# Kernel optimization log

Hardware: AMD Instinct MI355X
Metric: run time of the kernel (lower is better)

The kernel has to match this reference:

```python
import jax, jax.numpy as jnp
import numpy as np

N, E, IN_DIM, OUT_DIM, H = 4096, 131072, 1024, 512, 4


def setup_inputs() -> dict:
    key = jax.random.key(0)
    k1, k2, k3, k4 = jax.random.split(key, 4)
    x = jax.random.normal(k1, (N, IN_DIM), dtype=jnp.float32)
    edge_index = jax.random.randint(k2, (2, E), 0, N, dtype=jnp.int64)
    # learned params, scaled like torch Linear init (~1/sqrt(fan_in))
    W = jax.random.normal(k3, (H, IN_DIM, OUT_DIM), dtype=jnp.float32) * 0.02
    a = jax.random.normal(k4, (H, 2 * OUT_DIM), dtype=jnp.float32) * 0.02
    return {"x": x, "edge_index": edge_index, "W": W, "a": a}


def reference(x, edge_index, W, a):
    row, col = edge_index[0], edge_index[1]
    n = x.shape[0]
    h = jnp.einsum('ni,hio->hno', x, W)                    # [H, N, out]
    # per-edge attention logits: a . [h[row] || h[col]]
    a_src, a_dst = a[:, :OUT_DIM], a[:, OUT_DIM:]
    e = (jnp.einsum('heo,ho->he', h[:, row], a_src)
         + jnp.einsum('heo,ho->he', h[:, col], a_dst))      # [H, E]
    e = jnp.where(e > 0, e, 0.2 * e)                        # LeakyReLU(0.2)
    # dense NxN attention matrix exactly as the original (zeros at non-edges
    # DO participate in the row softmax, matching the torch code)
    att = jnp.zeros((H, n, n), dtype=h.dtype).at[:, row, col].set(e)
    att = jax.nn.softmax(att, axis=-1)
    h_prime = jnp.einsum('hnm,hmo->hno', att, h)            # [H, N, out]
    return jnp.transpose(h_prime, (1, 0, 2)).reshape(n, H * OUT_DIM)
```

## Files before the change

### kernel.cpp

```cpp
#include <hip/hip_runtime.h>
#include <stdint.h>

#define NN 4096
#define EE 131072
#define IND 1024
#define OUTD 512
#define NH 4
#define NBKT 8
#define BKT_SHIFT 9

typedef __bf16 bf16x8 __attribute__((ext_vector_type(8)));
typedef float f32x4 __attribute__((ext_vector_type(4)));
typedef float f32x2 __attribute__((ext_vector_type(2)));

__device__ __forceinline__ unsigned short f2bf(float f) {
  unsigned u = __float_as_uint(f);
  u += 0x7FFFu + ((u >> 16) & 1u);
  return (unsigned short)(u >> 16);
}

__global__ void prep_edge_kernel(const float* __restrict__ x, unsigned short* __restrict__ xb,
                                 const float* __restrict__ W, unsigned short* __restrict__ Wt,
                                 const int* __restrict__ ei, unsigned* __restrict__ bitmap,
                                 int* __restrict__ counts2, unsigned char* __restrict__ flags) {
  __shared__ float tile[32][33];
  const int bid = blockIdx.x, t = threadIdx.x;
  if (bid < 4096) {
    int i = bid * 256 + t;
    float4 v = ((const float4*)x)[i];
    ushort4 o;
    o.x = f2bf(v.x); o.y = f2bf(v.y); o.z = f2bf(v.z); o.w = f2bf(v.w);
    ((ushort4*)xb)[i] = o;
  } else if (bid < 6144) {
    int b2 = bid - 4096;
    int i0 = (b2 & 31) * 32, o0 = ((b2 >> 5) & 15) * 32, h = b2 >> 9;
    int tx = t & 31, ty = t >> 5;
#pragma unroll
    for (int r = 0; r < 32; r += 8)
      tile[ty + r][tx] = W[((size_t)(h * IND + i0 + ty + r)) * OUTD + o0 + tx];
    __syncthreads();
#pragma unroll
    for (int r = 0; r < 32; r += 8)
      Wt[((size_t)(h * OUTD + o0 + ty + r)) * IND + i0 + tx] = f2bf(tile[tx][ty + r]);
  } else {
    int e = (bid - 6144) * 256 + t;
    int row = ei[e], col = ei[EE + e];
    unsigned key = ((unsigned)row << 12) | (unsigned)col;
    unsigned bit = 1u << (key & 31);
    unsigned old = atomicOr(&bitmap[key >> 5], bit);
    if (old & bit) { flags[e] = 1; return; }
    flags[e] = 0;
    atomicAdd(&counts2[row * NBKT + (col >> BKT_SHIFT)], 1);
  }
}

__device__ __forceinline__ void gload16(const unsigned short* g, unsigned short* l) {
  __builtin_amdgcn_global_load_lds((const __attribute__((address_space(1))) void*)g,
                                   (__attribute__((address_space(3))) void*)l, 16, 0, 0);
}

__device__ void scan_block_256(const int* __restrict__ c2, int* __restrict__ off2,
                               int* __restrict__ cur2) {
  __shared__ int wtot[4];
  const int t = threadIdx.x, w = t >> 6, lane = t & 63;
  const int4* src = (const int4*)c2 + t * 32;
  int s = 0;
  for (int k = 0; k < 32; k++) { int4 v = src[k]; s += v.x + v.y + v.z + v.w; }
  int inc = s;
#pragma unroll
  for (int d = 1; d < 64; d <<= 1) {
    int u = __shfl_up(inc, d);
    if (lane >= d) inc += u;
  }
  if (lane == 63) wtot[w] = inc;
  __syncthreads();
  int wpre = 0;
#pragma unroll
  for (int k = 0; k < 4; k++)
    if (k < w) wpre += wtot[k];
  int o = wpre + inc - s;
  if (t == 255) off2[NN * NBKT] = o + s;
  int4* od = (int4*)off2 + t * 32;
  int4* cd = (int4*)cur2 + t * 32;
  for (int k = 0; k < 32; k++) {
    int4 v = src[k];
    int4 ov;
    ov.x = o; o += v.x;
    ov.y = o; o += v.y;
    ov.z = o; o += v.z;
    ov.w = o; o += v.w;
    od[k] = ov;
    cd[k] = ov;
  }
}

__global__ __launch_bounds__(256, 4) void gemm_scan_kernel(
    const unsigned short* __restrict__ X, const unsigned short* __restrict__ Wt,
    const float* __restrict__ Av, unsigned char* __restrict__ Hb8,
    float* __restrict__ s4_src, float* __restrict__ s4_dst, float* __restrict__ Scol,
    const int* __restrict__ c2, int* __restrict__ off2, int* __restrict__ cur2) {
  if (blockIdx.x == 512) {
    scan_block_256(c2, off2, cur2);
    return;
  }
  __shared__ __align__(16) unsigned short As[2][4096];
  __shared__ __align__(16) unsigned short Bs[2][4096];
  const int t = threadIdx.x, w = t >> 6, lane = t & 63;
  const int bx = blockIdx.x & 3, hh = (blockIdx.x >> 2) & 3, by = blockIdx.x >> 4;

  const unsigned short* Ab0 = X + (size_t)(by * 128) * IND;
  const unsigned short* Bb0 = Wt + (size_t)(hh * OUTD + bx * 128) * IND;

  const int seg0 = w * 128 + lane, seg1 = w * 128 + 64 + lane;
  const int sr0 = seg0 >> 2, sc0 = (seg0 & 3) ^ ((sr0 >> 1) & 3);
  const int sr1 = seg1 >> 2, sc1 = (seg1 & 3) ^ ((sr1 >> 1) & 3);

  const int wr = w >> 1, wc = w & 1, g = lane >> 4, rlo = lane & 15;
  int aoff[4], boff[4];
#pragma unroll
  for (int i = 0; i < 4; i++) {
    int ra = wr * 64 + i * 16 + rlo;
    aoff[i] = ra * 64 + ((g ^ ((ra >> 1) & 3)) << 4);
    int rb = wc * 64 + i * 16 + rlo;
    boff[i] = rb * 64 + ((g ^ ((rb >> 1) & 3)) << 4);
  }

  f32x4 zero = {0.f, 0.f, 0.f, 0.f};
  f32x4 acc[4][4];
#pragma unroll
  for (int i = 0; i < 4; i++)
#pragma unroll
    for (int j = 0; j < 4; j++) acc[i][j] = zero;

#define STAGE(buf, kt)                                               \
  do {                                                               \
    const unsigned short* ga = Ab0 + (kt) * 32;                      \
    const unsigned short* gb = Bb0 + (kt) * 32;                      \
    gload16(ga + sr0 * IND + sc0 * 8, &As[buf][w * 1024]);           \
    gload16(ga + sr1 * IND + sc1 * 8, &As[buf][w * 1024 + 512]);     \
    gload16(gb + sr0 * IND + sc0 * 8, &Bs[buf][w * 1024]);           \
    gload16(gb + sr1 * IND + sc1 * 8, &Bs[buf][w * 1024 + 512]);     \
  } while (0)

  STAGE(0, 0);
  __syncthreads();
  int cur = 0;
  for (int kt = 0; kt < 32; ++kt) {
    if (kt != 31) STAGE(cur ^ 1, kt + 1);
    const char* Abuf = (const char*)As[cur];
    const char* Bbuf = (const char*)Bs[cur];
    bf16x8 av[4], bv[4];
#pragma unroll
    for (int i = 0; i < 4; i++) {
      av[i] = *(const bf16x8*)(Abuf + aoff[i]);
      bv[i] = *(const bf16x8*)(Bbuf + boff[i]);
    }
#pragma unroll
    for (int i = 0; i < 4; i++)
#pragma unroll
      for (int j = 0; j < 4; j++)
        acc[i][j] = __builtin_amdgcn_mfma_f32_16x16x32_bf16(av[i], bv[j], acc[i][j], 0, 0, 0);
    __syncthreads();
    cur ^= 1;
  }
#undef STAGE

#pragma unroll
  for (int i = 0; i < 4; i++)
#pragma unroll
    for (int j = 0; j < 4; j++) {
      int mm0 = by * 128 + wr * 64 + i * 16 + g * 4;
      int nn = bx * 128 + wc * 64 + j * 16 + rlo;
#pragma unroll
      for (int q = 0; q < 4; q++) {
        int p = __builtin_amdgcn_cvt_pk_fp8_f32(acc[i][j][q], acc[i][j][q], 0, false);
        Hb8[((size_t)(mm0 + q) * NH + hh) * OUTD + nn] = (unsigned char)p;
      }
    }

  float as_[4], ad_[4];
#pragma unroll
  for (int j = 0; j < 4; j++) {
    int nn = bx * 128 + wc * 64 + j * 16 + rlo;
    as_[j] = Av[hh * 2 * OUTD + nn];
    ad_[j] = Av[hh * 2 * OUTD + OUTD + nn];
  }
#pragma unroll
  for (int i = 0; i < 4; i++)
#pragma unroll
    for (int q = 0; q < 4; q++) {
      float vs = 0.f, vd = 0.f;
#pragma unroll
      for (int j = 0; j < 4; j++) {
        float tv = acc[i][j][q];
        vs += tv * as_[j];
        vd += tv * ad_[j];
      }
#pragma unroll
      for (int m = 1; m < 16; m <<= 1) {
        vs += __shfl_xor(vs, m);
        vd += __shfl_xor(vd, m);
      }
      if (rlo == 0) {
        int r = by * 128 + wr * 64 + i * 16 + g * 4 + q;
        atomicAdd(&s4_src[r * NH + hh], vs);
        atomicAdd(&s4_dst[r * NH + hh], vd);
      }
    }

#pragma unroll
  for (int j = 0; j < 4; j++) {
    float cv = 0.f;
#pragma unroll
    for (int i = 0; i < 4; i++)
#pragma unroll
      for (int q = 0; q < 4; q++) cv += acc[i][j][q];
    cv += __shfl_xor(cv, 16);
    cv += __shfl_xor(cv, 32);
    if (g == 0) {
      int nn = bx * 128 + wc * 64 + j * 16 + rlo;
      atomicAdd(&Scol[hh * OUTD + nn], cv);
    }
  }
}

__global__ void edge_b_kernel(const int* __restrict__ ei, const unsigned char* __restrict__ flags,
                              int* __restrict__ cursor2, int* __restrict__ csr_col) {
  int e = blockIdx.x * 256 + threadIdx.x;
  if (flags[e]) return;
  int row = ei[e], col = ei[EE + e];
  int pos = atomicAdd(&cursor2[row * NBKT + (col >> BKT_SHIFT)], 1);
  csr_col[pos] = col;
}

__global__ __launch_bounds__(256) void finalize_kernel(
    const unsigned char* __restrict__ Hb8,
    const float* __restrict__ S, const float* __restrict__ s4_src,
    const float* __restrict__ s4_dst, const int* __restrict__ offsets2,
    const int* __restrict__ csr_col, float* __restrict__ out) {
  __shared__ int cols_s[64];
  __shared__ float g_s[4][64];
  const int i = blockIdx.x, t = threadIdx.x;
  const int w = t >> 6, lane = t & 63;

  const float ssrc = s4_src[i * NH + w];
  float acc[8];
  {
    const float4* Sv = (const float4*)(S + w * OUTD + lane * 8);
    float4 s0 = Sv[0], s1 = Sv[1];
    acc[0] = s0.x; acc[1] = s0.y; acc[2] = s0.z; acc[3] = s0.w;
    acc[4] = s1.x; acc[5] = s1.y; acc[6] = s1.z; acc[7] = s1.w;
  }
  float gsum = 0.f;

  const int start = offsets2[i * NBKT];
  const int cnt = offsets2[(i + 1) * NBKT] - start;
  for (int base = 0; base < cnt; base += 64) {
    int nload = min(64, cnt - base);
    __syncthreads();
    if (w == 0) cols_s[lane] = (lane < nload) ? csr_col[start + base + lane] : 0;
    __syncthreads();
    {
      float gg = 0.f;
      if (lane < nload) {
        float e0 = ssrc + s4_dst[cols_s[lane] * NH + w];
        e0 = e0 > 0.f ? e0 : 0.2f * e0;
        gg = expf(e0) - 1.0f;
      }
      g_s[w][lane] = gg;
    }
#pragma unroll 4
    for (int k = 0; k < nload; k++) {
      int cc = cols_s[k];
      float gg = g_s[w][k];
      gsum += gg;
      uint2 u = *(const uint2*)(Hb8 + ((size_t)(cc * NH + w)) * OUTD + lane * 8);
      f32x2 p0 = __builtin_amdgcn_cvt_pk_f32_fp8(u.x, false);
      f32x2 p1 = __builtin_amdgcn_cvt_pk_f32_fp8(u.x, true);
      f32x2 p2 = __builtin_amdgcn_cvt_pk_f32_fp8(u.y, false);
      f32x2 p3 = __builtin_amdgcn_cvt_pk_f32_fp8(u.y, true);
      acc[0] += gg * p0[0];
      acc[1] += gg * p0[1];
      acc[2] += gg * p1[0];
      acc[3] += gg * p1[1];
      acc[4] += gg * p2[0];
      acc[5] += gg * p2[1];
      acc[6] += gg * p3[0];
      acc[7] += gg * p3[1];
    }
  }

  float inv = 1.0f / ((float)NN + gsum);
  float4 o0, o1;
  o0.x = acc[0] * inv; o0.y = acc[1] * inv; o0.z = acc[2] * inv; o0.w = acc[3] * inv;
  o1.x = acc[4] * inv; o1.y = acc[5] * inv; o1.z = acc[6] * inv; o1.w = acc[7] * inv;
  float* ob = out + (size_t)i * (NH * OUTD) + w * OUTD + lane * 8;
  ((float4*)ob)[0] = o0;
  ((float4*)ob)[1] = o1;
}

extern "C" void kernel_launch(void* const* d_in, const int* in_sizes, int n_in,
                              void* d_out, int out_size, void* d_ws, size_t ws_size,
                              hipStream_t stream) {
  const float* x = (const float*)d_in[0];
  const int* ei = (const int*)d_in[1];
  const float* W = (const float*)d_in[2];
  const float* a = (const float*)d_in[3];
  float* out = (float*)d_out;

  char* ws = (char*)d_ws;
  unsigned short* xb = (unsigned short*)(ws);
  unsigned short* wt = (unsigned short*)(ws + (8ull << 20));
  unsigned char* Hb8 = (unsigned char*)(ws + (12ull << 20));
  char* zreg = ws + (20ull << 20);
  float* s4_src = (float*)(zreg);
  float* s4_dst = (float*)(zreg + 65536);
  float* Scol = (float*)(zreg + 2 * 65536);
  int* counts2 = (int*)(zreg + 2 * 65536 + 8192);
  unsigned* bitmap = (unsigned*)(zreg + 2 * 65536 + 8192 + 131072);
  const size_t ZBYTES = 2 * 65536 + 8192 + 131072 + ((size_t)NN * NN / 8);
  unsigned char* flags = (unsigned char*)(ws + (23ull << 20));
  int* offsets2 = (int*)(ws + (23ull << 20) + 262144);
  int* cursor2 = (int*)(ws + (23ull << 20) + 2 * 262144);
  int* csr_col = (int*)(ws + (24ull << 20));

  hipMemsetAsync(zreg, 0, ZBYTES, stream);

  prep_edge_kernel<<<4096 + 2048 + 512, 256, 0, stream>>>(x, xb, W, wt, ei, bitmap, counts2,
                                                          flags);
  gemm_scan_kernel<<<513, 256, 0, stream>>>(xb, wt, a, Hb8, s4_src, s4_dst, Scol, counts2,
                                            offsets2, cursor2);
  edge_b_kernel<<<EE / 256, 256, 0, stream>>>(ei, flags, cursor2, csr_col);
  finalize_kernel<<<NN, 256, 0, stream>>>(Hb8, Scol, s4_src, s4_dst, offsets2, csr_col, out);
}
```

Baseline: 182.5 us.

## Double GEMM K-tile to 64 with 8-way swizzle and refine column buckets

The GEMM K-tile grows from 32 to 64, with a new 8-column XOR swizzle on the LDS layout. This halves the number of loop iterations and block barriers, at the cost of twice the shared memory and lower occupancy (launch bounds drop from 4 to 2). Separately, the per-row column buckets grow from 8 to 16, with the scan and workspace offsets adjusted to match. This presumably gives the finalize kernel finer-grained bucketing, but it enlarges the counts, offsets and cursor arrays that must be zeroed and scanned.

```diff
diff --git a/kernel.cpp b/kernel.cpp
--- a/kernel.cpp
+++ b/kernel.cpp
@@ -6,8 +6,8 @@
 #define IND 1024
 #define OUTD 512
 #define NH 4
-#define NBKT 8
-#define BKT_SHIFT 9
+#define NBKT 16
+#define BKT_SHIFT 8
 
 typedef __bf16 bf16x8 __attribute__((ext_vector_type(8)));
 typedef float f32x4 __attribute__((ext_vector_type(4)));
@@ -63,9 +63,9 @@
                                int* __restrict__ cur2) {
   __shared__ int wtot[4];
   const int t = threadIdx.x, w = t >> 6, lane = t & 63;
-  const int4* src = (const int4*)c2 + t * 32;
+  const int4* src = (const int4*)c2 + t * 64;
   int s = 0;
-  for (int k = 0; k < 32; k++) { int4 v = src[k]; s += v.x + v.y + v.z + v.w; }
+  for (int k = 0; k < 64; k++) { int4 v = src[k]; s += v.x + v.y + v.z + v.w; }
   int inc = s;
 #pragma unroll
   for (int d = 1; d < 64; d <<= 1) {
@@ -80,9 +80,9 @@
     if (k < w) wpre += wtot[k];
   int o = wpre + inc - s;
   if (t == 255) off2[NN * NBKT] = o + s;
-  int4* od = (int4*)off2 + t * 32;
-  int4* cd = (int4*)cur2 + t * 32;
-  for (int k = 0; k < 32; k++) {
+  int4* od = (int4*)off2 + t * 64;
+  int4* cd = (int4*)cur2 + t * 64;
+  for (int k = 0; k < 64; k++) {
     int4 v = src[k];
     int4 ov;
     ov.x = o; o += v.x;
@@ -94,7 +94,7 @@
   }
 }
 
-__global__ __launch_bounds__(256, 4) void gemm_scan_kernel(
+__global__ __launch_bounds__(256, 2) void gemm_scan_kernel(
     const unsigned short* __restrict__ X, const unsigned short* __restrict__ Wt,
     const float* __restrict__ Av, unsigned char* __restrict__ Hb8,
     float* __restrict__ s4_src, float* __restrict__ s4_dst, float* __restrict__ Scol,
@@ -103,27 +103,33 @@
     scan_block_256(c2, off2, cur2);
     return;
   }
-  __shared__ __align__(16) unsigned short As[2][4096];
-  __shared__ __align__(16) unsigned short Bs[2][4096];
+  __shared__ __align__(16) unsigned short As[2][8192];
+  __shared__ __align__(16) unsigned short Bs[2][8192];
   const int t = threadIdx.x, w = t >> 6, lane = t & 63;
   const int bx = blockIdx.x & 3, hh = (blockIdx.x >> 2) & 3, by = blockIdx.x >> 4;
 
   const unsigned short* Ab0 = X + (size_t)(by * 128) * IND;
   const unsigned short* Bb0 = Wt + (size_t)(hh * OUTD + bx * 128) * IND;
 
-  const int seg0 = w * 128 + lane, seg1 = w * 128 + 64 + lane;
-  const int sr0 = seg0 >> 2, sc0 = (seg0 & 3) ^ ((sr0 >> 1) & 3);
-  const int sr1 = seg1 >> 2, sc1 = (seg1 & 3) ^ ((sr1 >> 1) & 3);
+  int srowA[4], scgA[4];
+#pragma unroll
+  for (int k = 0; k < 4; k++) {
+    int seg = w * 64 + k * 256 + lane;
+    srowA[k] = seg >> 3;
+    scgA[k] = (seg & 7) ^ (srowA[k] & 7);
+  }
 
   const int wr = w >> 1, wc = w & 1, g = lane >> 4, rlo = lane & 15;
-  int aoff[4], boff[4];
-#pragma unroll
-  for (int i = 0; i < 4; i++) {
-    int ra = wr * 64 + i * 16 + rlo;
-    aoff[i] = ra * 64 + ((g ^ ((ra >> 1) & 3)) << 4);
-    int rb = wc * 64 + i * 16 + rlo;
-    boff[i] = rb * 64 + ((g ^ ((rb >> 1) & 3)) << 4);
-  }
+  int aoff[4][2], boff[4][2];
+#pragma unroll
+  for (int i = 0; i < 4; i++)
+#pragma unroll
+    for (int ki = 0; ki < 2; ki++) {
+      int ra = wr * 64 + i * 16 + rlo;
+      aoff[i][ki] = ra * 128 + (((ki * 4 + g) ^ (ra & 7)) << 4);
+      int rb = wc * 64 + i * 16 + rlo;
+      boff[i][ki] = rb * 128 + (((ki * 4 + g) ^ (rb & 7)) << 4);
+    }
 
   f32x4 zero = {0.f, 0.f, 0.f, 0.f};
   f32x4 acc[4][4];
@@ -132,34 +138,39 @@
 #pragma unroll
     for (int j = 0; j < 4; j++) acc[i][j] = zero;
 
-#define STAGE(buf, kt)                                               \
-  do {                                                               \
-    const unsigned short* ga = Ab0 + (kt) * 32;                      \
-    const unsigned short* gb = Bb0 + (kt) * 32;                      \
-    gload16(ga + sr0 * IND + sc0 * 8, &As[buf][w * 1024]);           \
-    gload16(ga + sr1 * IND + sc1 * 8, &As[buf][w * 1024 + 512]);     \
-    gload16(gb + sr0 * IND + sc0 * 8, &Bs[buf][w * 1024]);           \
-    gload16(gb + sr1 * IND + sc1 * 8, &Bs[buf][w * 1024 + 512]);     \
+#define STAGE(buf, kt)                                                       \
+  do {                                                                       \
+    const unsigned short* ga = Ab0 + (kt) * 64;                              \
+    const unsigned short* gb = Bb0 + (kt) * 64;                              \
+    _Pragma("unroll") for (int k = 0; k < 4; k++) {                          \
+      gload16(ga + srowA[k] * IND + scgA[k] * 8, &As[buf][(w * 64 + k * 256) * 8]); \
+      gload16(gb + srowA[k] * IND + scgA[k] * 8, &Bs[buf][(w * 64 + k * 256) * 8]); \
+    }                                                                        \
   } while (0)
 
   STAGE(0, 0);
   __syncthreads();
   int cur = 0;
-  for (int kt = 0; kt < 32; ++kt) {
-    if (kt != 31) STAGE(cur ^ 1, kt + 1);
+  for (int kt = 0; kt < 16; ++kt) {
+    if (kt != 15) STAGE(cur ^ 1, kt + 1);
     const char* Abuf = (const char*)As[cur];
     const char* Bbuf = (const char*)Bs[cur];
-    bf16x8 av[4], bv[4];
-#pragma unroll
-    for (int i = 0; i < 4; i++) {
-      av[i] = *(const bf16x8*)(Abuf + aoff[i]);
-      bv[i] = *(const bf16x8*)(Bbuf + boff[i]);
-    }
+    bf16x8 av[4][2], bv[4][2];
 #pragma unroll
     for (int i = 0; i < 4; i++)
 #pragma unroll
-      for (int j = 0; j < 4; j++)
-        acc[i][j] = __builtin_amdgcn_mfma_f32_16x16x32_bf16(av[i], bv[j], acc[i][j], 0, 0, 0);
+      for (int ki = 0; ki < 2; ki++) {
+        av[i][ki] = *(const bf16x8*)(Abuf + aoff[i][ki]);
+        bv[i][ki] = *(const bf16x8*)(Bbuf + boff[i][ki]);
+      }
+#pragma unroll
+    for (int ki = 0; ki < 2; ki++)
+#pragma unroll
+      for (int i = 0; i < 4; i++)
+#pragma unroll
+        for (int j = 0; j < 4; j++)
+          acc[i][j] =
+              __builtin_amdgcn_mfma_f32_16x16x32_bf16(av[i][ki], bv[j][ki], acc[i][j], 0, 0, 0);
     __syncthreads();
     cur ^= 1;
   }
@@ -317,11 +328,11 @@
   float* s4_dst = (float*)(zreg + 65536);
   float* Scol = (float*)(zreg + 2 * 65536);
   int* counts2 = (int*)(zreg + 2 * 65536 + 8192);
-  unsigned* bitmap = (unsigned*)(zreg + 2 * 65536 + 8192 + 131072);
-  const size_t ZBYTES = 2 * 65536 + 8192 + 131072 + ((size_t)NN * NN / 8);
+  unsigned* bitmap = (unsigned*)(zreg + 2 * 65536 + 8192 + 262144);
+  const size_t ZBYTES = 2 * 65536 + 8192 + 262144 + ((size_t)NN * NN / 8);
   unsigned char* flags = (unsigned char*)(ws + (23ull << 20));
   int* offsets2 = (int*)(ws + (23ull << 20) + 262144);
-  int* cursor2 = (int*)(ws + (23ull << 20) + 2 * 262144);
+  int* cursor2 = (int*)(ws + (23ull << 20) + 262144 + 524288);
   int* csr_col = (int*)(ws + (24ull << 20));
 
   hipMemsetAsync(zreg, 0, ZBYTES, stream);
```

Result: slower. 199.1 us (+9.1%).
